# Optimization experiments

Measured on AMD Instinct MI355X. Metric: run time of the kernel, lower is better.

## Reference

```python
import jax, jax.numpy as jnp
import numpy as np

B = 131072      # batch of states
N_ACT = 40      # output_dim (Tetris action space)


def setup_inputs() -> dict:
    key = jax.random.key(0)
    ks = jax.random.split(key, 9)
    # state vector: 11 real-valued board features, 1 hold-piece id in [0,4),
    # 3 next-piece ids in [1,8) (0 is treated as invalid by the original code)
    keep = jax.random.normal(ks[0], (B, 11), dtype=jnp.float32)
    hold = jax.random.randint(ks[1], (B, 1), 0, 4).astype(jnp.float32)
    nxt = jax.random.randint(ks[2], (B, 3), 1, 8).astype(jnp.float32)
    x = jnp.concatenate([keep, hold, nxt], axis=1)  # [B, 15]
    W1 = jax.random.normal(ks[3], (36, 128), dtype=jnp.float32) * 0.1
    b1 = jnp.zeros((128,), dtype=jnp.float32)
    W2 = jax.random.normal(ks[4], (128, 512), dtype=jnp.float32) * 0.05
    b2 = jnp.zeros((512,), dtype=jnp.float32)
    W4 = jax.random.normal(ks[5], (512, N_ACT), dtype=jnp.float32) * 0.05
    b4 = jnp.zeros((N_ACT,), dtype=jnp.float32)
    return {"x": x, "W1": W1, "b1": b1, "W2": W2, "b2": b2, "W4": W4, "b4": b4}


def reference(x, W1, b1, W2, b2, W4, b4):
    B_, _ = x.shape
    keep = x[:, :11]                                      # [B, 11]
    # vectorized replacement of the per-sample .item() one-hot loop
    hold_idx = jax.lax.stop_gradient(jnp.clip(x[:, 11].astype(jnp.int32), 0, 3))
    nxt_idx = jax.lax.stop_gradient(jnp.clip(x[:, 12:15].astype(jnp.int32) - 1, 0, 6))
    hold_oh = jax.nn.one_hot(hold_idx, 4, dtype=x.dtype)  # [B, 4]
    nxt_oh = jax.nn.one_hot(nxt_idx, 7, dtype=x.dtype).reshape(B_, 21)  # [B, 21]
    inp = jnp.concatenate([keep, hold_oh, nxt_oh], axis=1)  # [B, 36]
    h = jax.nn.relu(inp @ W1 + b1)   # [B, 128]
    h = jax.nn.relu(h @ W2 + b2)     # [B, 512]
    return h @ W4 + b4               # [B, N_ACT]
```

## Files before the change

### kernel.cpp

```cpp
#include <hip/hip_runtime.h>


typedef short bf16x8 __attribute__((ext_vector_type(8)));
typedef float f32x4 __attribute__((ext_vector_type(4)));
typedef unsigned int u32;

#define NW1F 8192
#define NW2F 65536
#define NW4F 24576
#define PACK_TOTAL (NW1F + NW2F + NW4F)

__device__ __forceinline__ unsigned short f2bf(float f) {
  union { float f; unsigned u; } a; a.f = f;
  unsigned r = a.u + 0x7fffu + ((a.u >> 16) & 1u);
  return (unsigned short)(r >> 16);
}
__device__ __forceinline__ u32 pack2bf(float a, float b) {
  return (u32)f2bf(a) | ((u32)f2bf(b) << 16);
}

__global__ void pack_weights(const float* __restrict__ W1,
                             const float* __restrict__ W2,
                             const float* __restrict__ W4,
                             unsigned short* __restrict__ wf) {
  int id = blockIdx.x * 256 + threadIdx.x;
  if (id >= PACK_TOTAL) return;
  int rem = id & 511, lane = rem >> 3, j = rem & 7;
  int l16 = lane & 15, quad = lane >> 4;
  if (id < NW1F) {
    int frag = id >> 9;
    int mt = frag >> 1, ks = frag & 1;
    int m = mt * 16 + l16, k = ks * 32 + quad * 8 + j;
    wf[id] = f2bf(k < 36 ? W1[k * 128 + m] : 0.f);
  } else if (id < NW1F + NW2F) {
    int frag = (id - NW1F) >> 9;
    int mt = frag >> 2, ks = frag & 3;
    int m = mt * 16 + l16, k = ks * 32 + quad * 8 + j;
    wf[id] = f2bf(W2[k * 512 + m]);
  } else {
    int frag = (id - NW1F - NW2F) >> 9;
    int mt = frag >> 4, ks = frag & 15;
    int m = mt * 16 + l16, k = ks * 32 + quad * 8 + j;
    wf[id] = f2bf(m < 40 ? W4[k * 40 + m] : 0.f);
  }
}

__global__ __launch_bounds__(256, 3) void dqn_fused(
    const float* __restrict__ x,
    const unsigned short* __restrict__ wf,
    const float* __restrict__ b1,
    const float* __restrict__ b2,
    const float* __restrict__ b4,
    float* __restrict__ out) {
  __shared__ __align__(16) unsigned short sU[4 * 32 * 72];
  __shared__ __align__(16) unsigned short sH1[4 * 32 * 136];

  const int tid  = threadIdx.x;
  const int lane = tid & 63;
  const int wave = tid >> 6;
  const int quad = lane >> 4;
  const int l16  = lane & 15;
  const int row0 = blockIdx.x << 7;
  const int lr0  = wave * 32;
  unsigned short* su  = sU  + wave * (32 * 72);
  unsigned short* sh1 = sH1 + wave * (32 * 136);

  if (lane < 32) {
    const float* xr = x + (size_t)(row0 + lr0 + lane) * 15;
    unsigned short* dst = su + lane * 72;
    bf16x8 z = {0, 0, 0, 0, 0, 0, 0, 0};
#pragma unroll
    for (int c = 8; c < 64; c += 8) *(bf16x8*)(dst + c) = z;
    u32 p[4];
#pragma unroll
    for (int i = 0; i < 4; ++i) p[i] = pack2bf(xr[2 * i], xr[2 * i + 1]);
    *(bf16x8*)dst = *(bf16x8*)p;
    *(u32*)(dst + 8) = pack2bf(xr[8], xr[9]);
    dst[10] = f2bf(xr[10]);
    int hold = (int)xr[11]; hold = hold < 0 ? 0 : (hold > 3 ? 3 : hold);
    dst[11 + hold] = 0x3F80;
#pragma unroll
    for (int t = 0; t < 3; ++t) {
      int nx = (int)xr[12 + t] - 1; nx = nx < 0 ? 0 : (nx > 6 ? 6 : nx);
      dst[15 + t * 7 + nx] = 0x3F80;
    }
  }

  const f32x4 vzero = {0.f, 0.f, 0.f, 0.f};

  bf16x8 ib[2][2];
#pragma unroll
  for (int rg = 0; rg < 2; ++rg)
#pragma unroll
    for (int ks = 0; ks < 2; ++ks)
      ib[rg][ks] = *(const bf16x8*)(su + (rg * 16 + l16) * 72 + ks * 32 + quad * 8);

  f32x4 acc1[8][2];
#pragma unroll
  for (int mt = 0; mt < 8; ++mt) { acc1[mt][0] = vzero; acc1[mt][1] = vzero; }
#pragma unroll
  for (int mt = 0; mt < 8; ++mt)
#pragma unroll
    for (int ks = 0; ks < 2; ++ks) {
      bf16x8 wa = *(const bf16x8*)(wf + (size_t)((mt * 2 + ks) * 64 + lane) * 8);
      acc1[mt][0] = __builtin_amdgcn_mfma_f32_16x16x32_bf16(wa, ib[0][ks], acc1[mt][0], 0, 0, 0);
      acc1[mt][1] = __builtin_amdgcn_mfma_f32_16x16x32_bf16(wa, ib[1][ks], acc1[mt][1], 0, 0, 0);
    }
#pragma unroll
  for (int mt = 0; mt < 8; ++mt) {
    f32x4 bias = *(const f32x4*)(b1 + mt * 16 + quad * 4);
#pragma unroll
    for (int rg = 0; rg < 2; ++rg) {
      float v0 = fmaxf(acc1[mt][rg][0] + bias[0], 0.f);
      float v1 = fmaxf(acc1[mt][rg][1] + bias[1], 0.f);
      float v2 = fmaxf(acc1[mt][rg][2] + bias[2], 0.f);
      float v3 = fmaxf(acc1[mt][rg][3] + bias[3], 0.f);
      u32 p0 = pack2bf(v0, v1), p1 = pack2bf(v2, v3);
      uint2 pk = {p0, p1};
      *(uint2*)(sh1 + (rg * 16 + l16) * 136 + mt * 16 + quad * 4) = pk;
    }
  }

  bf16x8 af1[2][4];
#pragma unroll
  for (int rg = 0; rg < 2; ++rg)
#pragma unroll
    for (int ks = 0; ks < 4; ++ks)
      af1[rg][ks] = *(const bf16x8*)(sh1 + (rg * 16 + l16) * 136 + ks * 32 + quad * 8);

  f32x4 accO[3][2];
#pragma unroll
  for (int mt = 0; mt < 3; ++mt) { accO[mt][0] = vzero; accO[mt][1] = vzero; }

  const unsigned short* w2f = wf + NW1F;
  const unsigned short* w4f = wf + NW1F + NW2F;

  for (int chunk = 0; chunk < 8; ++chunk) {
    f32x4 acc2[4][2];
#pragma unroll
    for (int mtl = 0; mtl < 4; ++mtl) { acc2[mtl][0] = vzero; acc2[mtl][1] = vzero; }

#pragma unroll
    for (int ks = 0; ks < 4; ++ks)
#pragma unroll
      for (int mtl = 0; mtl < 4; ++mtl) {
        bf16x8 w = *(const bf16x8*)(w2f + (size_t)((((chunk * 4 + mtl) * 4) + ks) * 64 + lane) * 8);
        acc2[mtl][0] = __builtin_amdgcn_mfma_f32_16x16x32_bf16(w, af1[0][ks], acc2[mtl][0], 0, 0, 0);
        acc2[mtl][1] = __builtin_amdgcn_mfma_f32_16x16x32_bf16(w, af1[1][ks], acc2[mtl][1], 0, 0, 0);
      }
#pragma unroll
    for (int mtl = 0; mtl < 4; ++mtl) {
      f32x4 bias = *(const f32x4*)(b2 + chunk * 64 + mtl * 16 + quad * 4);
#pragma unroll
      for (int rg = 0; rg < 2; ++rg) {
        float v0 = fmaxf(acc2[mtl][rg][0] + bias[0], 0.f);
        float v1 = fmaxf(acc2[mtl][rg][1] + bias[1], 0.f);
        float v2 = fmaxf(acc2[mtl][rg][2] + bias[2], 0.f);
        float v3 = fmaxf(acc2[mtl][rg][3] + bias[3], 0.f);
        uint2 pk = {pack2bf(v0, v1), pack2bf(v2, v3)};
        *(uint2*)(su + (rg * 16 + l16) * 72 + mtl * 16 + quad * 4) = pk;
      }
    }
#pragma unroll
    for (int ks3 = 0; ks3 < 2; ++ks3) {
      bf16x8 h0 = *(const bf16x8*)(su + (l16)      * 72 + ks3 * 32 + quad * 8);
      bf16x8 h1f = *(const bf16x8*)(su + (16 + l16) * 72 + ks3 * 32 + quad * 8);
#pragma unroll
      for (int mt3 = 0; mt3 < 3; ++mt3) {
        bf16x8 w = *(const bf16x8*)(w4f + (size_t)((mt3 * 16 + chunk * 2 + ks3) * 64 + lane) * 8);
        accO[mt3][0] = __builtin_amdgcn_mfma_f32_16x16x32_bf16(w, h0,  accO[mt3][0], 0, 0, 0);
        accO[mt3][1] = __builtin_amdgcn_mfma_f32_16x16x32_bf16(w, h1f, accO[mt3][1], 0, 0, 0);
      }
    }
  }

#pragma unroll
  for (int mt3 = 0; mt3 < 3; ++mt3) {
    int colbase = mt3 * 16 + quad * 4;
    if (colbase < 40) {
      f32x4 bias = *(const f32x4*)(b4 + colbase);
#pragma unroll
      for (int rg = 0; rg < 2; ++rg) {
        f32x4 v = accO[mt3][rg] + bias;
        size_t row = (size_t)(row0 + lr0 + rg * 16 + l16);
        *(f32x4*)(out + row * 40 + colbase) = v;
      }
    }
  }
}

extern "C" void kernel_launch(void* const* d_in, const int* in_sizes, int n_in,
                              void* d_out, int out_size, void* d_ws, size_t ws_size,
                              hipStream_t stream) {
  const float* x  = (const float*)d_in[0];
  const float* W1 = (const float*)d_in[1];
  const float* b1 = (const float*)d_in[2];
  const float* W2 = (const float*)d_in[3];
  const float* b2 = (const float*)d_in[4];
  const float* W4 = (const float*)d_in[5];
  const float* b4 = (const float*)d_in[6];
  float* out = (float*)d_out;
  unsigned short* wf = (unsigned short*)d_ws;

  int B = in_sizes[0] / 15;

  hipLaunchKernelGGL(pack_weights, dim3((PACK_TOTAL + 255) / 256), dim3(256), 0, stream,
                     W1, W2, W4, wf);
  hipLaunchKernelGGL(dqn_fused, dim3(B / 128), dim3(256), 0, stream,
                     x, wf, b1, b2, b4, out);
}
```

Measured before the change: 114.6 us.

## Alias LDS buffers for higher occupancy and use hardware bf16 pack conversion

The separate input and hidden-1 LDS buffers are merged into one per-wave buffer that is reused across layers. This cuts shared memory per block so launch bounds can rise from 3 to 4 blocks per CU, aiming to hide memory latency better. The software round-to-nearest bf16 packing is replaced by the v_cvt_pk_bf16_f32 instruction. The weight-packing kernel is also changed to have each thread produce 8 bf16 values and issue one vector store. The buffer reuse relies on each wave finishing its reads before it overwrites the same buffer, and the higher occupancy target may push the compiler into register pressure or spills.

```diff
diff --git a/kernel.cpp b/kernel.cpp
--- a/kernel.cpp
+++ b/kernel.cpp
@@ -9,51 +9,58 @@
 #define NW2F 65536
 #define NW4F 24576
 #define PACK_TOTAL (NW1F + NW2F + NW4F)
+#define PACK_THREADS (PACK_TOTAL / 8)
 
 __device__ __forceinline__ unsigned short f2bf(float f) {
   union { float f; unsigned u; } a; a.f = f;
   unsigned r = a.u + 0x7fffu + ((a.u >> 16) & 1u);
   return (unsigned short)(r >> 16);
 }
-__device__ __forceinline__ u32 pack2bf(float a, float b) {
-  return (u32)f2bf(a) | ((u32)f2bf(b) << 16);
+__device__ __forceinline__ u32 cvtpk(float lo, float hi) {
+  u32 r;
+  asm("v_cvt_pk_bf16_f32 %0, %1, %2" : "=v"(r) : "v"(lo), "v"(hi));
+  return r;
 }
 
 __global__ void pack_weights(const float* __restrict__ W1,
                              const float* __restrict__ W2,
                              const float* __restrict__ W4,
                              unsigned short* __restrict__ wf) {
-  int id = blockIdx.x * 256 + threadIdx.x;
-  if (id >= PACK_TOTAL) return;
-  int rem = id & 511, lane = rem >> 3, j = rem & 7;
+  int t = blockIdx.x * 256 + threadIdx.x;
+  if (t >= PACK_THREADS) return;
+  int fid = t >> 6, lane = t & 63;
   int l16 = lane & 15, quad = lane >> 4;
-  if (id < NW1F) {
-    int frag = id >> 9;
-    int mt = frag >> 1, ks = frag & 1;
-    int m = mt * 16 + l16, k = ks * 32 + quad * 8 + j;
-    wf[id] = f2bf(k < 36 ? W1[k * 128 + m] : 0.f);
-  } else if (id < NW1F + NW2F) {
-    int frag = (id - NW1F) >> 9;
-    int mt = frag >> 2, ks = frag & 3;
-    int m = mt * 16 + l16, k = ks * 32 + quad * 8 + j;
-    wf[id] = f2bf(W2[k * 512 + m]);
+  float vals[8];
+  if (fid < 16) {
+    int mt = fid >> 1, ks = fid & 1;
+    int m = mt * 16 + l16, k0 = ks * 32 + quad * 8;
+#pragma unroll
+    for (int j = 0; j < 8; ++j) { int k = k0 + j; vals[j] = (k < 36) ? W1[k * 128 + m] : 0.f; }
+  } else if (fid < 144) {
+    int f = fid - 16, mt = f >> 2, ks = f & 3;
+    int m = mt * 16 + l16, k0 = ks * 32 + quad * 8;
+#pragma unroll
+    for (int j = 0; j < 8; ++j) vals[j] = W2[(k0 + j) * 512 + m];
   } else {
-    int frag = (id - NW1F - NW2F) >> 9;
-    int mt = frag >> 4, ks = frag & 15;
-    int m = mt * 16 + l16, k = ks * 32 + quad * 8 + j;
-    wf[id] = f2bf(m < 40 ? W4[k * 40 + m] : 0.f);
-  }
-}
-
-__global__ __launch_bounds__(256, 3) void dqn_fused(
+    int f = fid - 144, mt = f >> 4, ks = f & 15;
+    int m = mt * 16 + l16, k0 = ks * 32 + quad * 8;
+#pragma unroll
+    for (int j = 0; j < 8; ++j) vals[j] = (m < 40) ? W4[(k0 + j) * 40 + m] : 0.f;
+  }
+  u32 p[4];
+#pragma unroll
+  for (int j = 0; j < 4; ++j) p[j] = cvtpk(vals[2 * j], vals[2 * j + 1]);
+  *(bf16x8*)(wf + (size_t)t * 8) = *(bf16x8*)p;
+}
+
+__global__ __launch_bounds__(256, 4) void dqn_fused(
     const float* __restrict__ x,
     const unsigned short* __restrict__ wf,
     const float* __restrict__ b1,
     const float* __restrict__ b2,
     const float* __restrict__ b4,
     float* __restrict__ out) {
-  __shared__ __align__(16) unsigned short sU[4 * 32 * 72];
-  __shared__ __align__(16) unsigned short sH1[4 * 32 * 136];
+  __shared__ __align__(16) unsigned short sBuf[4 * 4352];
 
   const int tid  = threadIdx.x;
   const int lane = tid & 63;
@@ -62,8 +69,7 @@
   const int l16  = lane & 15;
   const int row0 = blockIdx.x << 7;
   const int lr0  = wave * 32;
-  unsigned short* su  = sU  + wave * (32 * 72);
-  unsigned short* sh1 = sH1 + wave * (32 * 136);
+  unsigned short* su = sBuf + wave * 4352;
 
   if (lane < 32) {
     const float* xr = x + (size_t)(row0 + lr0 + lane) * 15;
@@ -73,9 +79,9 @@
     for (int c = 8; c < 64; c += 8) *(bf16x8*)(dst + c) = z;
     u32 p[4];
 #pragma unroll
-    for (int i = 0; i < 4; ++i) p[i] = pack2bf(xr[2 * i], xr[2 * i + 1]);
+    for (int i = 0; i < 4; ++i) p[i] = cvtpk(xr[2 * i], xr[2 * i + 1]);
     *(bf16x8*)dst = *(bf16x8*)p;
-    *(u32*)(dst + 8) = pack2bf(xr[8], xr[9]);
+    *(u32*)(dst + 8) = cvtpk(xr[8], xr[9]);
     dst[10] = f2bf(xr[10]);
     int hold = (int)xr[11]; hold = hold < 0 ? 0 : (hold > 3 ? 3 : hold);
     dst[11 + hold] = 0x3F80;
@@ -115,9 +121,8 @@
       float v1 = fmaxf(acc1[mt][rg][1] + bias[1], 0.f);
       float v2 = fmaxf(acc1[mt][rg][2] + bias[2], 0.f);
       float v3 = fmaxf(acc1[mt][rg][3] + bias[3], 0.f);
-      u32 p0 = pack2bf(v0, v1), p1 = pack2bf(v2, v3);
-      uint2 pk = {p0, p1};
-      *(uint2*)(sh1 + (rg * 16 + l16) * 136 + mt * 16 + quad * 4) = pk;
+      uint2 pk = {cvtpk(v0, v1), cvtpk(v2, v3)};
+      *(uint2*)(su + (rg * 16 + l16) * 136 + mt * 16 + quad * 4) = pk;
     }
   }
 
@@ -126,7 +131,7 @@
   for (int rg = 0; rg < 2; ++rg)
 #pragma unroll
     for (int ks = 0; ks < 4; ++ks)
-      af1[rg][ks] = *(const bf16x8*)(sh1 + (rg * 16 + l16) * 136 + ks * 32 + quad * 8);
+      af1[rg][ks] = *(const bf16x8*)(su + (rg * 16 + l16) * 136 + ks * 32 + quad * 8);
 
   f32x4 accO[3][2];
 #pragma unroll
@@ -157,13 +162,13 @@
         float v1 = fmaxf(acc2[mtl][rg][1] + bias[1], 0.f);
         float v2 = fmaxf(acc2[mtl][rg][2] + bias[2], 0.f);
         float v3 = fmaxf(acc2[mtl][rg][3] + bias[3], 0.f);
-        uint2 pk = {pack2bf(v0, v1), pack2bf(v2, v3)};
+        uint2 pk = {cvtpk(v0, v1), cvtpk(v2, v3)};
         *(uint2*)(su + (rg * 16 + l16) * 72 + mtl * 16 + quad * 4) = pk;
       }
     }
 #pragma unroll
     for (int ks3 = 0; ks3 < 2; ++ks3) {
-      bf16x8 h0 = *(const bf16x8*)(su + (l16)      * 72 + ks3 * 32 + quad * 8);
+      bf16x8 h0  = *(const bf16x8*)(su + (l16)      * 72 + ks3 * 32 + quad * 8);
       bf16x8 h1f = *(const bf16x8*)(su + (16 + l16) * 72 + ks3 * 32 + quad * 8);
 #pragma unroll
       for (int mt3 = 0; mt3 < 3; ++mt3) {
@@ -204,7 +209,7 @@
 
   int B = in_sizes[0] / 15;
 
-  hipLaunchKernelGGL(pack_weights, dim3((PACK_TOTAL + 255) / 256), dim3(256), 0, stream,
+  hipLaunchKernelGGL(pack_weights, dim3((PACK_THREADS + 255) / 256), dim3(256), 0, stream,
                      W1, W2, W4, wf);
   hipLaunchKernelGGL(dqn_fused, dim3(B / 128), dim3(256), 0, stream,
                      x, wf, b1, b2, b4, out);
```

Result: slower. 123.4 us (+7.7%).
